# Kernel tuning notes

Hardware: AMD Instinct MI355X
Metric: run time of the kernel (lower is better)

The kernel has to match this reference:

```python
import jax, jax.numpy as jnp
import numpy as np

B, N, HID, NH, NREL, E = 4, 1024, 768, 12, 64, 65536
DH = HID // NH  # 64
TOKEN_TYPE = 0  # NodeType.TOKEN.value


def setup_inputs() -> dict:
    key = jax.random.key(0)
    ks = jax.random.split(key, 24)
    s = 0.02
    inp = {}
    inp["node_states"] = jax.random.normal(ks[0], (B, N, HID), jnp.float32)
    eb = jax.random.randint(ks[1], (E,), 0, B)
    eh = jax.random.randint(ks[2], (E,), 0, N)
    et = jax.random.randint(ks[3], (E,), 0, N)
    er = jax.random.randint(ks[4], (E,), 0, NREL)
    inp["edge_indices"] = jnp.stack([eb, eh, et, er]).astype(jnp.int32)
    inp["node_type_ids"] = jax.random.randint(ks[5], (B, N), 0, 3).astype(jnp.int32)
    names = ["Wq", "Wk", "Wv", "Wq_kb", "Wk_kb", "Wv_kb"]
    for i, nm in enumerate(names):
        inp[nm] = jax.random.normal(ks[6 + i], (HID, HID), jnp.float32) * s
        inp["b" + nm[1:]] = jax.random.normal(ks[12 + i], (HID,), jnp.float32) * s
    inp["rel_mats"] = jax.random.normal(ks[18], (NREL, DH, DH), jnp.float32) * s
    edge_emb = jax.random.normal(ks[19], (NREL, HID), jnp.float32) * s
    inp["edge_emb"] = edge_emb.at[0].set(0.0)  # TOKEN_TO_TOKEN_RELATION_ID row zeroed
    return inp


def reference(node_states, edge_indices, node_type_ids,
              Wq, bq, Wk, bk, Wv, bv,
              Wq_kb, bq_kb, Wk_kb, bk_kb, Wv_kb, bv_kb,
              rel_mats, edge_emb):
    eb, eh, et, er = edge_indices  # (E,) each
    tok = (node_type_ids == TOKEN_TYPE)[..., None]  # (B, N, 1)

    def dual(W_tok, b_tok, W_kb, b_kb):
        # mask_a * tok_proj(x) + mask_b * kb_proj(x)
        return jnp.where(tok, node_states @ W_tok.T + b_tok,
                         node_states @ W_kb.T + b_kb)

    Q = dual(Wq, bq, Wq_kb, bq_kb)  # (B, N, HID)
    K = dual(Wk, bk, Wk_kb, bk_kb)
    V = dual(Wv, bv, Wv_kb, bv_kb)

    # --- attention logits on edges ---
    Qe = Q[eb, eh].reshape(E, NH, DH)  # query at head node
    Ke = K[eb, et].reshape(E, NH, DH)  # key at tail node
    Me = rel_mats[er]                  # (E, DH, DH) per-edge relation matrix
    # (Q @ M) . K per head, scaled
    logits = jnp.einsum('ehd,edf,ehf->eh', Qe, Me, Ke) / jnp.sqrt(
        jnp.asarray(DH, node_states.dtype))  # (E, NH)

    # --- sparse softmax over tail nodes, per (batch, head_node, att_head) ---
    seg = eb * N + eh  # (E,)
    mx = jax.ops.segment_max(logits, seg, num_segments=B * N)  # (B*N, NH)
    ex = jnp.exp(logits - mx[seg])
    denom = jax.ops.segment_sum(ex, seg, num_segments=B * N)
    probs = ex / denom[seg]  # (E, NH); dropout p=0.0 (eval)

    # --- values: V at tail node + edge value embedding ---
    Ve = (V[eb, et] + edge_emb[er]).reshape(E, NH, DH)

    # --- weighted scatter-sum over tail dim ---
    msg = probs[..., None] * Ve  # (E, NH, DH)
    out = jax.ops.segment_sum(msg, seg, num_segments=B * N)  # (B*N, NH, DH)
    return out.reshape(B, N, HID)
```

## Files before the change

kernel.cpp:

```cpp
#include <hip/hip_runtime.h>
#include <math.h>
#include <stdint.h>

#define BB   4
#define NN   1024
#define HID  768
#define NH   12
#define DH   64
#define NREL 64
#define EE   65536
#define NSEG (BB*NN)
#define NOUT 4608
#define UNIT_E 64
#define MAXU (EE/UNIT_E + NREL)
#define NBLK 256
#define MAXMT 34

typedef __bf16 bf16;
typedef __bf16 bf16x8 __attribute__((ext_vector_type(8)));
typedef float  f32x4  __attribute__((ext_vector_type(4)));

__device__ __forceinline__ void load_lds16(const void* g, void* l) {
  __builtin_amdgcn_global_load_lds(
      (__attribute__((address_space(1))) void*)(uintptr_t)g,
      (__attribute__((address_space(3))) void*)(uintptr_t)l, 16, 0, 0);
}

__device__ __forceinline__ int swz(int byte_off) {
  return byte_off ^ (((byte_off >> 7) & 7) << 4);
}

__device__ __forceinline__ float b2f(unsigned short u) {
  return __uint_as_float(((unsigned)u) << 16);
}

__global__ __launch_bounds__(1024)
void partition_kernel(const int* __restrict__ nt, int* __restrict__ origrow,
                      int* __restrict__ meta){
  __shared__ int sums[1024];
  __shared__ int ntot;
  const int t = threadIdx.x;
  int tk[4]; int c = 0;
  #pragma unroll
  for (int i=0;i<4;i++){ tk[i] = (nt[t*4+i]==0); c += tk[i]; }
  sums[t]=c; __syncthreads();
  for (int off=1; off<1024; off<<=1){
    const int v = (t>=off) ? sums[t-off] : 0;
    __syncthreads();
    sums[t]+=v;
    __syncthreads();
  }
  if (t==1023) ntot = sums[1023];
  __syncthreads();
  const int excl = sums[t]-c;
  int tokpos = excl, kbpos = ntot + (4*t - excl);
  #pragma unroll
  for (int i=0;i<4;i++){
    if (tk[i]) origrow[tokpos++] = t*4+i;
    else       origrow[kbpos++]  = t*4+i;
  }
  if (t==0){
    const int ntok = ntot, nkb = NSEG - ntok;
    const int tt = (ntok+127)>>7, ktt = (nkb+127)>>7;
    meta[0]=ntok; meta[1]=tt+ktt;
    for (int m=0;m<tt+ktt;m++){
      meta[2+m]  = (m<tt) ? m*128 : ntok + (m-tt)*128;
      meta[40+m] = (m<tt) ? 1 : 0;
    }
  }
}

__global__ __launch_bounds__(256)
void prep_kernel(const float* __restrict__ X, const int* __restrict__ origrow,
                 const float* __restrict__ W0, const float* __restrict__ W1,
                 const float* __restrict__ W2, const float* __restrict__ W3,
                 const float* __restrict__ W4, const float* __restrict__ W5,
                 const float* __restrict__ b0, const float* __restrict__ b1,
                 const float* __restrict__ b2, const float* __restrict__ b3,
                 const float* __restrict__ b4, const float* __restrict__ b5,
                 const float* __restrict__ relm,
                 bf16* __restrict__ Xp, bf16* __restrict__ Wb,
                 float* __restrict__ biasAll, bf16* __restrict__ Mt){
  const int blk = blockIdx.x, tid = threadIdx.x;
  if (blk < NSEG) {
    if (tid < 192) {
      const int orig = origrow[blk];
      float4 v = *reinterpret_cast<const float4*>(X + (size_t)orig*HID + tid*4);
      bf16 o[4] = {(bf16)v.x,(bf16)v.y,(bf16)v.z,(bf16)v.w};
      *reinterpret_cast<uint64_t*>(Xp + (size_t)blk*HID + tid*4) = *reinterpret_cast<uint64_t*>(o);
    }
  } else if (blk < NSEG + NOUT) {
    const int r = blk - NSEG;
    const int j = r / HID;
    const int o = r - j * HID;
    const float* Wj; const float* bj;
    if      (j==0){Wj=W0;bj=b0;} else if(j==1){Wj=W1;bj=b1;}
    else if (j==2){Wj=W2;bj=b2;} else if(j==3){Wj=W3;bj=b3;}
    else if (j==4){Wj=W4;bj=b4;} else            {Wj=W5;bj=b5;}
    const float* src = Wj + (size_t)o * HID;
    bf16* dst = Wb + (size_t)r * HID;
    for (int c = tid; c < HID; c += 256) dst[c] = (bf16)src[c];
    if (tid == 0) biasAll[r] = bj[o];
  } else {
    const int r = blk - NSEG - NOUT;
    const float* M = relm + (size_t)r * DH * DH;
    bf16* o = Mt + (size_t)r * DH * DH;
    for (int i = tid; i < DH * DH; i += 256) {
      const int d = i >> 6, f = i & 63;
      o[f * DH + d] = (bf16)M[i];
    }
  }
}

#define BM 128
#define BN 128
#define BK 32
#define NT (HID/BK)

__global__ __launch_bounds__(256)
void gemm_kernel(const bf16* __restrict__ A, const bf16* __restrict__ Bw,
                 const float* __restrict__ biasAll, const int* __restrict__ origrow,
                 const int* __restrict__ meta,
                 bf16* __restrict__ Qb, bf16* __restrict__ Kb, bf16* __restrict__ Vb)
{
  __shared__ bf16 As[2][BM * BK];
  __shared__ bf16 Bs[2][BN * BK];
  const int mt = blockIdx.x;
  const int ntok = meta[0], nmt = meta[1];
  if (mt >= nmt) return;
  const int base  = meta[2+mt];
  const int istok = meta[40+mt];

  const int tid  = threadIdx.x;
  const int lane = tid & 63;
  const int w    = tid >> 6;
  const int wrow = w >> 1, wcol = w & 1;
  const int ct_local = blockIdx.y * BN;
  const int brow0 = (istok ? 0 : 2304) + ct_local;

  f32x4 acc[4][4];
  #pragma unroll
  for (int mi=0;mi<4;mi++)
    #pragma unroll
    for (int ni=0;ni<4;ni++) acc[mi][ni] = (f32x4){0.f,0.f,0.f,0.f};

  const char* Ab = (const char*)A;
  const char* Bb = (const char*)Bw;

  int rowg[2], inrowg[2], Pg[2];
  #pragma unroll
  for (int i = 0; i < 2; ++i) {
    const int e = i * 256 + tid;
    const int P = e * 16;
    const int L = swz(P);
    Pg[i] = P; rowg[i] = L >> 6; inrowg[i] = L & 63;
  }

  #define STAGE(kt, b)                                                              \
    { _Pragma("unroll")                                                             \
      for (int i = 0; i < 2; ++i) {                                                 \
        load_lds16(Ab + ((size_t)(base  + rowg[i]) * HID + (kt) * BK) * 2 + inrowg[i], \
                   (char*)As[b] + Pg[i]);                                           \
        load_lds16(Bb + ((size_t)(brow0 + rowg[i]) * HID + (kt) * BK) * 2 + inrowg[i], \
                   (char*)Bs[b] + Pg[i]);                                           \
      } }

  STAGE(0, 0);

  for (int kt = 0; kt < NT; ++kt) {
    __syncthreads();
    if (kt + 1 < NT) STAGE(kt + 1, (kt + 1) & 1);

    const char* Asb = (const char*)As[kt & 1];
    const char* Bsb = (const char*)Bs[kt & 1];
    bf16x8 af[4], bfr[4];
    #pragma unroll
    for (int mi = 0; mi < 4; ++mi) {
      const int r = wrow * 64 + mi * 16 + (lane & 15);
      const int L = r * 64 + (lane >> 4) * 16;
      af[mi] = *reinterpret_cast<const bf16x8*>(Asb + swz(L));
    }
    #pragma unroll
    for (int ni = 0; ni < 4; ++ni) {
      const int r = wcol * 64 + ni * 16 + (lane & 15);
      const int L = r * 64 + (lane >> 4) * 16;
      bfr[ni] = *reinterpret_cast<const bf16x8*>(Bsb + swz(L));
    }
    #pragma unroll
    for (int mi = 0; mi < 4; ++mi)
      #pragma unroll
      for (int ni = 0; ni < 4; ++ni)
        acc[mi][ni] = __builtin_amdgcn_mfma_f32_16x16x32_bf16(af[mi], bfr[ni], acc[mi][ni], 0, 0, 0);
  }

  const int j3 = ct_local / HID;
  const int o0 = ct_local - j3 * HID;
  const int rowLim = istok ? ntok : NSEG;
  const int bidx0 = (istok ? j3 : j3 + 3) * HID + o0;
  #pragma unroll
  for (int mi = 0; mi < 4; ++mi) {
    #pragma unroll
    for (int i = 0; i < 4; ++i) {
      const int rr = base + wrow * 64 + mi * 16 + (lane >> 4) * 4 + i;
      if (rr < rowLim) {
        const int orig = origrow[rr];
        #pragma unroll
        for (int ni = 0; ni < 4; ++ni) {
          const int cg = wcol * 64 + ni * 16 + (lane & 15);
          const float val = acc[mi][ni][i] + biasAll[bidx0 + cg];
          if (j3 == 2)      Vb[(size_t)orig * HID + o0 + cg] = (bf16)val;
          else if (j3 == 0) Qb[(size_t)orig * HID + o0 + cg] = (bf16)val;
          else              Kb[(size_t)orig * HID + o0 + cg] = (bf16)val;
        }
      }
    }
  }
}

__global__ __launch_bounds__(256)
void hist_both_kernel(const int* __restrict__ ei, int* __restrict__ cnt,
                      int* __restrict__ cnt_blk){
  __shared__ int lc[NREL];
  const int tid = threadIdx.x, blk = blockIdx.x;
  if (tid < NREL) lc[tid] = 0;
  __syncthreads();
  const int e = blk*256 + tid;
  atomicAdd(&cnt[ei[e]*NN + ei[EE+e]], 1);
  atomicAdd(&lc[ei[3*EE+e]], 1);
  __syncthreads();
  if (tid < NREL) cnt_blk[tid*NBLK + blk] = lc[tid];
}

__global__ __launch_bounds__(1024)
void scan_both_kernel(const int* __restrict__ cnt, int* __restrict__ start,
                      int* __restrict__ cursor, int* __restrict__ cnt_blk,
                      int* __restrict__ start_rel, int* __restrict__ cnt_rel,
                      int* __restrict__ ustart){
  __shared__ int sums[1024];
  const int t = threadIdx.x;
  if (blockIdx.x == 0) {
    const int c0=cnt[t*4], c1=cnt[t*4+1], c2=cnt[t*4+2], c3=cnt[t*4+3];
    const int s = c0+c1+c2+c3;
    sums[t]=s; __syncthreads();
    for (int off=1; off<1024; off<<=1){
      const int v = (t>=off) ? sums[t-off] : 0;
      __syncthreads();
      sums[t]+=v;
      __syncthreads();
    }
    const int excl = sums[t]-s;
    const int o0=excl, o1=o0+c0, o2=o1+c1, o3=o2+c2;
    start[t*4]=o0;  start[t*4+1]=o1;  start[t*4+2]=o2;  start[t*4+3]=o3;
    cursor[t*4]=o0; cursor[t*4+1]=o1; cursor[t*4+2]=o2; cursor[t*4+3]=o3;
  } else {
    int v[16]; int s = 0;
    #pragma unroll
    for (int i=0;i<16;i++){ v[i] = cnt_blk[t*16+i]; s += v[i]; }
    sums[t] = s; __syncthreads();
    for (int off=1; off<1024; off<<=1){
      const int x = (t>=off) ? sums[t-off] : 0;
      __syncthreads();
      sums[t] += x;
      __syncthreads();
    }
    int run = sums[t] - s;
    #pragma unroll
    for (int i=0;i<16;i++){ const int c = v[i]; cnt_blk[t*16+i] = run; run += c; }
    __syncthreads();
    if (t < NREL) {
      const int st  = cnt_blk[t*NBLK];
      const int nxt = (t == NREL-1) ? EE : cnt_blk[(t+1)*NBLK];
      const int c   = nxt - st;
      start_rel[t] = st;
      cnt_rel[t]   = c;
      const int units = (c + UNIT_E - 1) / UNIT_E;
      int su = units;
      #pragma unroll
      for (int off=1; off<64; off<<=1) {
        const int vu = __shfl_up(su, off);
        if (t >= off) su += vu;
      }
      ustart[t] = su - units;
      if (t == NREL-1) ustart[NREL] = su;
    }
  }
}

__global__ __launch_bounds__(256)
void scatter_both_kernel(const int* __restrict__ ei, int* __restrict__ cursor,
                         int* __restrict__ order, const int* __restrict__ base_blk,
                         int* __restrict__ order_rel){
  __shared__ int lc[NREL];
  const int tid = threadIdx.x, blk = blockIdx.x;
  if (tid < NREL) lc[tid] = 0;
  __syncthreads();
  const int e = blk*256 + tid;
  const int seg = ei[e]*NN + ei[EE+e];
  order[atomicAdd(&cursor[seg], 1)] = e;
  const int r = ei[3*EE + e];
  const int rank = atomicAdd(&lc[r], 1);
  order_rel[base_blk[r*NBLK + blk] + rank] = e;
}

__global__ __launch_bounds__(256)
void logits_mfma_kernel(const bf16* __restrict__ Qb, const bf16* __restrict__ Kb,
                        const int* __restrict__ ei, const bf16* __restrict__ Mt,
                        const int* __restrict__ order_rel, const int* __restrict__ start_rel,
                        const int* __restrict__ cnt_rel, const int* __restrict__ ustart,
                        float* __restrict__ L)
{
  __shared__ int qoff[UNIT_E], koff[UNIT_E], eidx[UNIT_E];
  __shared__ int us[NREL+1];
  __shared__ int relsh;
  const int tid = threadIdx.x;
  const int u = blockIdx.x;
  if (tid < NREL+1) us[tid] = ustart[tid];
  __syncthreads();
  if (u >= us[NREL]) return;
  if (tid < NREL && us[tid] <= u && u < us[tid+1]) relsh = tid;
  __syncthreads();
  const int r = relsh;
  const int lu = u - us[r];
  const int ebase = start_rel[r] + lu * UNIT_E;
  const int nvalid = min(UNIT_E, cnt_rel[r] - lu * UNIT_E);
  if (tid < UNIT_E) {
    const int epos = ebase + (tid < nvalid ? tid : 0);
    const int e = order_rel[epos];
    eidx[tid] = (tid < nvalid) ? e : -1;
    const int eb = ei[e], eh = ei[EE+e], et = ei[2*EE+e];
    qoff[tid] = (eb*NN + eh) * HID;
    koff[tid] = (eb*NN + et) * HID;
  }
  __syncthreads();

  const int w = tid >> 6, lane = tid & 63;
  const int l15 = lane & 15, lg = lane >> 4;
  const bf16* Mr = Mt + (size_t)r * DH * DH;
  bf16x8 bfr[4][2];
  #pragma unroll
  for (int ni = 0; ni < 4; ++ni)
    #pragma unroll
    for (int kk = 0; kk < 2; ++kk)
      bfr[ni][kk] = *reinterpret_cast<const bf16x8*>(
          Mr + (ni*16 + l15) * DH + kk*32 + lg*8);

  #define LOADQ(mt, a0, a1)                                              \
    { const int lr = (mt)*16 + l15;                                      \
      const int el = lr / 12, hh = lr - el*12;                           \
      const int qo = qoff[w*16 + el] + hh*64 + lg*8;                     \
      a0 = *reinterpret_cast<const bf16x8*>(Qb + qo);                    \
      a1 = *reinterpret_cast<const bf16x8*>(Qb + qo + 32); }

  #define LOADK(mt, kr)                                                  \
    { _Pragma("unroll")                                                  \
      for (int i = 0; i < 4; ++i) {                                      \
        const int lr2 = (mt)*16 + lg*4 + i;                              \
        const int el2 = lr2 / 12, h2 = lr2 - el2*12;                     \
        const int ko = koff[w*16 + el2] + h2*64 + l15;                   \
        _Pragma("unroll")                                                \
        for (int ni = 0; ni < 4; ++ni)                                   \
          kr[i*4+ni] = *reinterpret_cast<const unsigned short*>(Kb + ko + ni*16); } }

  #define COMPUTE(mt, a0, a1, kr)                                        \
    { f32x4 acc_[4];                                                     \
      _Pragma("unroll")                                                  \
      for (int ni = 0; ni < 4; ++ni) {                                   \
        acc_[ni] = (f32x4){0.f,0.f,0.f,0.f};                             \
        acc_[ni] = __builtin_amdgcn_mfma_f32_16x16x32_bf16(a0, bfr[ni][0], acc_[ni], 0, 0, 0); \
        acc_[ni] = __builtin_amdgcn_mfma_f32_16x16x32_bf16(a1, bfr[ni][1], acc_[ni], 0, 0, 0); \
      }                                                                  \
      _Pragma("unroll")                                                  \
      for (int i = 0; i < 4; ++i) {                                      \
        const int lr2 = (mt)*16 + lg*4 + i;                              \
        const int el2 = lr2 / 12, h2 = lr2 - el2*12;                     \
        float p = acc_[0][i]*b2f(kr[i*4+0]) + acc_[1][i]*b2f(kr[i*4+1])  \
                + acc_[2][i]*b2f(kr[i*4+2]) + acc_[3][i]*b2f(kr[i*4+3]); \
        p += __shfl_xor(p, 1); p += __shfl_xor(p, 2);                    \
        p += __shfl_xor(p, 4); p += __shfl_xor(p, 8);                    \
        if (l15 == 0) {                                                  \
          const int e = eidx[w*16 + el2];                                \
          if (e >= 0) L[(size_t)e*NH + h2] = p * 0.125f;                 \
        } } }

  bf16x8 a0A, a1A, a0B, a1B;
  unsigned short krA[16], krB[16];
  LOADQ(0, a0A, a1A); LOADK(0, krA);
  #pragma unroll
  for (int mt = 0; mt < 12; mt += 2) {
    LOADQ(mt+1, a0B, a1B); LOADK(mt+1, krB);
    COMPUTE(mt, a0A, a1A, krA);
    if (mt + 2 < 12) { LOADQ(mt+2, a0A, a1A); LOADK(mt+2, krA); }
    COMPUTE(mt+1, a0B, a1B, krB);
  }
  #undef LOADQ
  #undef LOADK
  #undef COMPUTE
}

#define SEGCAP 128
__global__ __launch_bounds__(256)
void segout_kernel(const int* __restrict__ ei, const bf16* __restrict__ Vb,
                   const float* __restrict__ emb, const float* __restrict__ L,
                   const int* __restrict__ start, const int* __restrict__ cnt,
                   const int* __restrict__ order, float* __restrict__ out)
{
  const int s = blockIdx.x, tid = threadIdx.x;
  float* o = out + (size_t)s*HID;
  const int n = cnt[s];
  if (n==0){ o[tid]=0.f; o[tid+256]=0.f; o[tid+512]=0.f; return; }

  __shared__ float denom[NH];
  __shared__ float inv[NH];
  const int st = start[s];
  const int eb = s >> 10;
  const int h0 = tid >> 6;

  if (tid<NH) denom[tid]=0.f;

  if (n <= SEGCAP) {
    __shared__ float pr[SEGCAP*NH];
    __shared__ int voffs[SEGCAP];
    __shared__ int eoffs[SEGCAP];
    if (tid < n) {
      const int e = order[st + tid];
      voffs[tid] = (eb*NN + ei[2*EE+e]) * HID;
      eoffs[tid] = ei[3*EE+e] * HID;
    }
    __syncthreads();
    for (int idx=tid; idx<n*NH; idx+=256){
      const int e = order[st + idx/NH];
      const float v = expf(L[(size_t)e*NH + idx - (idx/NH)*NH]);
      pr[idx] = v;
      atomicAdd(&denom[idx - (idx/NH)*NH], v);
    }
    __syncthreads();
    if (tid<NH) inv[tid] = 1.f/denom[tid];
    __syncthreads();
    const float i0=inv[h0], i1=inv[h0+4], i2=inv[h0+8];
    float a0=0.f, a1=0.f, a2=0.f;
    for (int i=0;i<n;i++){
      const bf16* vr = Vb + voffs[i];
      const float* erow = emb + eoffs[i];
      const float p0 = pr[i*NH+h0  ]*i0;
      const float p1 = pr[i*NH+h0+4]*i1;
      const float p2 = pr[i*NH+h0+8]*i2;
      a0 += p0*(b2f(*(const unsigned short*)(vr+tid    ))+erow[tid    ]);
      a1 += p1*(b2f(*(const unsigned short*)(vr+tid+256))+erow[tid+256]);
      a2 += p2*(b2f(*(const unsigned short*)(vr+tid+512))+erow[tid+512]);
    }
    o[tid]=a0; o[tid+256]=a1; o[tid+512]=a2;
  } else {
    __syncthreads();
    for (int i=tid; i<n*NH; i+=256){
      const int e = order[st + i/NH];
      atomicAdd(&denom[i - (i/NH)*NH], expf(L[(size_t)e*NH + i - (i/NH)*NH]));
    }
    __syncthreads();
    if (tid<NH) inv[tid] = 1.f/denom[tid];
    __syncthreads();
    const float i0=inv[h0], i1=inv[h0+4], i2=inv[h0+8];
    float a0=0.f, a1=0.f, a2=0.f;
    for (int i=0;i<n;i++){
      const int e  = order[st+i];
      const int et = ei[2*EE+e], er = ei[3*EE+e];
      const bf16* vr = Vb + (size_t)(eb*NN+et)*HID;
      const float* erow = emb + (size_t)er*HID;
      const float p0 = expf(L[(size_t)e*NH+h0  ])*i0;
      const float p1 = expf(L[(size_t)e*NH+h0+4])*i1;
      const float p2 = expf(L[(size_t)e*NH+h0+8])*i2;
      a0 += p0*(b2f(*(const unsigned short*)(vr+tid    ))+erow[tid    ]);
      a1 += p1*(b2f(*(const unsigned short*)(vr+tid+256))+erow[tid+256]);
      a2 += p2*(b2f(*(const unsigned short*)(vr+tid+512))+erow[tid+512]);
    }
    o[tid]=a0; o[tid+256]=a1; o[tid+512]=a2;
  }
}

extern "C" void kernel_launch(void* const* d_in, const int* in_sizes, int n_in,
                              void* d_out, int out_size, void* d_ws, size_t ws_size,
                              hipStream_t stream)
{
  const float* X  = (const float*)d_in[0];
  const int*   ei = (const int*)d_in[1];
  const int*   nt = (const int*)d_in[2];
  const float* W[6]; const float* bia[6];
  for (int j=0;j<6;j++){ W[j]=(const float*)d_in[3+2*j]; bia[j]=(const float*)d_in[4+2*j]; }
  const float* relm = (const float*)d_in[15];
  const float* emb  = (const float*)d_in[16];
  float* out = (float*)d_out;

  char* p = (char*)d_ws;
  bf16*  Qb = (bf16*)p;  p += (size_t)NSEG*HID*2;
  bf16*  Kb = (bf16*)p;  p += (size_t)NSEG*HID*2;
  bf16*  Vb = (bf16*)p;  p += (size_t)NSEG*HID*2;
  float* L  = (float*)p; p += (size_t)EE*NH*4;
  int* cnt      = (int*)p; p += NSEG*4;
  int* start    = (int*)p; p += NSEG*4;
  int* cursor   = (int*)p; p += NSEG*4;
  int* order    = (int*)p; p += (size_t)EE*4;
  int* cnt_blk    = (int*)p; p += NREL*NBLK*4;
  int* start_rel  = (int*)p; p += NREL*4;
  int* cnt_rel    = (int*)p; p += NREL*4;
  int* ustart     = (int*)p; p += (NREL+4)*4;
  int* order_rel  = (int*)p; p += (size_t)EE*4;
  int* origrow    = (int*)p; p += (NSEG+128)*4;
  int* meta       = (int*)p; p += 80*4;
  bf16* Xp = (bf16*)p;  p += (size_t)(NSEG+128)*HID*2;
  bf16* Wb = (bf16*)p;  p += (size_t)NOUT*HID*2;
  bf16* Mt = (bf16*)p;  p += (size_t)NREL*DH*DH*2;
  float* biasAll = (float*)p; p += NOUT*4;

  hipMemsetAsync(cnt, 0, NSEG*sizeof(int), stream);

  partition_kernel<<<1, 1024, 0, stream>>>(nt, origrow, meta);
  prep_kernel<<<NSEG + NOUT + NREL, 256, 0, stream>>>(X, origrow,
      W[0],W[1],W[2],W[3],W[4],W[5],
      bia[0],bia[1],bia[2],bia[3],bia[4],bia[5], relm, Xp, Wb, biasAll, Mt);
  gemm_kernel<<<dim3(MAXMT, 2304/BN), 256, 0, stream>>>(Xp, Wb, biasAll, origrow,
      meta, Qb, Kb, Vb);

  hist_both_kernel<<<NBLK, 256, 0, stream>>>(ei, cnt, cnt_blk);
  scan_both_kernel<<<2, 1024, 0, stream>>>(cnt, start, cursor, cnt_blk,
      start_rel, cnt_rel, ustart);
  scatter_both_kernel<<<NBLK, 256, 0, stream>>>(ei, cursor, order, cnt_blk, order_rel);

  logits_mfma_kernel<<<MAXU, 256, 0, stream>>>(Qb, Kb, ei, Mt, order_rel,
      start_rel, cnt_rel, ustart, L);
  segout_kernel<<<NSEG, 256, 0, stream>>>(ei, Vb, emb, L, start, cnt, order, out);
}
```

Before: 149.4 us.

## Shrink GEMM N-tile, fold cnt memset into partition, store edge embeddings as bf16

```diff
diff --git a/kernel.cpp b/kernel.cpp
--- a/kernel.cpp
+++ b/kernel.cpp
@@ -36,13 +36,13 @@
 
 __global__ __launch_bounds__(1024)
 void partition_kernel(const int* __restrict__ nt, int* __restrict__ origrow,
-                      int* __restrict__ meta){
+                      int* __restrict__ meta, int* __restrict__ cnt){
   __shared__ int sums[1024];
   __shared__ int ntot;
   const int t = threadIdx.x;
   int tk[4]; int c = 0;
   #pragma unroll
-  for (int i=0;i<4;i++){ tk[i] = (nt[t*4+i]==0); c += tk[i]; }
+  for (int i=0;i<4;i++){ tk[i] = (nt[t*4+i]==0); c += tk[i]; cnt[t*4+i] = 0; }
   sums[t]=c; __syncthreads();
   for (int off=1; off<1024; off<<=1){
     const int v = (t>=off) ? sums[t-off] : 0;
@@ -78,9 +78,10 @@
                  const float* __restrict__ b0, const float* __restrict__ b1,
                  const float* __restrict__ b2, const float* __restrict__ b3,
                  const float* __restrict__ b4, const float* __restrict__ b5,
-                 const float* __restrict__ relm,
+                 const float* __restrict__ relm, const float* __restrict__ emb,
                  bf16* __restrict__ Xp, bf16* __restrict__ Wb,
-                 float* __restrict__ biasAll, bf16* __restrict__ Mt){
+                 float* __restrict__ biasAll, bf16* __restrict__ Mt,
+                 bf16* __restrict__ Eb){
   const int blk = blockIdx.x, tid = threadIdx.x;
   if (blk < NSEG) {
     if (tid < 192) {
@@ -101,7 +102,7 @@
     bf16* dst = Wb + (size_t)r * HID;
     for (int c = tid; c < HID; c += 256) dst[c] = (bf16)src[c];
     if (tid == 0) biasAll[r] = bj[o];
-  } else {
+  } else if (blk < NSEG + NOUT + NREL) {
     const int r = blk - NSEG - NOUT;
     const float* M = relm + (size_t)r * DH * DH;
     bf16* o = Mt + (size_t)r * DH * DH;
@@ -109,11 +110,16 @@
       const int d = i >> 6, f = i & 63;
       o[f * DH + d] = (bf16)M[i];
     }
+  } else {
+    const int r = blk - NSEG - NOUT - NREL;
+    const float* src = emb + (size_t)r * HID;
+    bf16* dst = Eb + (size_t)r * HID;
+    for (int c = tid; c < HID; c += 256) dst[c] = (bf16)src[c];
   }
 }
 
 #define BM 128
-#define BN 128
+#define BN 64
 #define BK 32
 #define NT (HID/BK)
 
@@ -138,32 +144,33 @@
   const int ct_local = blockIdx.y * BN;
   const int brow0 = (istok ? 0 : 2304) + ct_local;
 
-  f32x4 acc[4][4];
+  f32x4 acc[4][2];
   #pragma unroll
   for (int mi=0;mi<4;mi++)
     #pragma unroll
-    for (int ni=0;ni<4;ni++) acc[mi][ni] = (f32x4){0.f,0.f,0.f,0.f};
+    for (int ni=0;ni<2;ni++) acc[mi][ni] = (f32x4){0.f,0.f,0.f,0.f};
 
   const char* Ab = (const char*)A;
   const char* Bb = (const char*)Bw;
 
-  int rowg[2], inrowg[2], Pg[2];
+  int rowgA[2], inrowgA[2], PgA[2];
   #pragma unroll
   for (int i = 0; i < 2; ++i) {
-    const int e = i * 256 + tid;
-    const int P = e * 16;
+    const int P = (i * 256 + tid) * 16;
     const int L = swz(P);
-    Pg[i] = P; rowg[i] = L >> 6; inrowg[i] = L & 63;
-  }
+    PgA[i] = P; rowgA[i] = L >> 6; inrowgA[i] = L & 63;
+  }
+  const int PB = tid * 16;
+  const int LB = swz(PB);
+  const int rowgB = LB >> 6, inrowgB = LB & 63;
 
   #define STAGE(kt, b)                                                              \
     { _Pragma("unroll")                                                             \
-      for (int i = 0; i < 2; ++i) {                                                 \
-        load_lds16(Ab + ((size_t)(base  + rowg[i]) * HID + (kt) * BK) * 2 + inrowg[i], \
-                   (char*)As[b] + Pg[i]);                                           \
-        load_lds16(Bb + ((size_t)(brow0 + rowg[i]) * HID + (kt) * BK) * 2 + inrowg[i], \
-                   (char*)Bs[b] + Pg[i]);                                           \
-      } }
+      for (int i = 0; i < 2; ++i)                                                   \
+        load_lds16(Ab + ((size_t)(base  + rowgA[i]) * HID + (kt) * BK) * 2 + inrowgA[i], \
+                   (char*)As[b] + PgA[i]);                                          \
+      load_lds16(Bb + ((size_t)(brow0 + rowgB) * HID + (kt) * BK) * 2 + inrowgB,    \
+                 (char*)Bs[b] + PB); }
 
   STAGE(0, 0);
 
@@ -173,7 +180,7 @@
 
     const char* Asb = (const char*)As[kt & 1];
     const char* Bsb = (const char*)Bs[kt & 1];
-    bf16x8 af[4], bfr[4];
+    bf16x8 af[4], bfr[2];
     #pragma unroll
     for (int mi = 0; mi < 4; ++mi) {
       const int r = wrow * 64 + mi * 16 + (lane & 15);
@@ -181,15 +188,15 @@
       af[mi] = *reinterpret_cast<const bf16x8*>(Asb + swz(L));
     }
     #pragma unroll
-    for (int ni = 0; ni < 4; ++ni) {
-      const int r = wcol * 64 + ni * 16 + (lane & 15);
+    for (int ni = 0; ni < 2; ++ni) {
+      const int r = wcol * 32 + ni * 16 + (lane & 15);
       const int L = r * 64 + (lane >> 4) * 16;
       bfr[ni] = *reinterpret_cast<const bf16x8*>(Bsb + swz(L));
     }
     #pragma unroll
     for (int mi = 0; mi < 4; ++mi)
       #pragma unroll
-      for (int ni = 0; ni < 4; ++ni)
+      for (int ni = 0; ni < 2; ++ni)
         acc[mi][ni] = __builtin_amdgcn_mfma_f32_16x16x32_bf16(af[mi], bfr[ni], acc[mi][ni], 0, 0, 0);
   }
 
@@ -205,8 +212,8 @@
       if (rr < rowLim) {
         const int orig = origrow[rr];
         #pragma unroll
-        for (int ni = 0; ni < 4; ++ni) {
-          const int cg = wcol * 64 + ni * 16 + (lane & 15);
+        for (int ni = 0; ni < 2; ++ni) {
+          const int cg = wcol * 32 + ni * 16 + (lane & 15);
           const float val = acc[mi][ni][i] + biasAll[bidx0 + cg];
           if (j3 == 2)      Vb[(size_t)orig * HID + o0 + cg] = (bf16)val;
           else if (j3 == 0) Qb[(size_t)orig * HID + o0 + cg] = (bf16)val;
@@ -400,7 +407,7 @@
 #define SEGCAP 128
 __global__ __launch_bounds__(256)
 void segout_kernel(const int* __restrict__ ei, const bf16* __restrict__ Vb,
-                   const float* __restrict__ emb, const float* __restrict__ L,
+                   const bf16* __restrict__ Eb, const float* __restrict__ L,
                    const int* __restrict__ start, const int* __restrict__ cnt,
                    const int* __restrict__ order, float* __restrict__ out)
 {
@@ -440,13 +447,13 @@
     float a0=0.f, a1=0.f, a2=0.f;
     for (int i=0;i<n;i++){
       const bf16* vr = Vb + voffs[i];
-      const float* erow = emb + eoffs[i];
+      const bf16* erow = Eb + eoffs[i];
       const float p0 = pr[i*NH+h0  ]*i0;
       const float p1 = pr[i*NH+h0+4]*i1;
       const float p2 = pr[i*NH+h0+8]*i2;
-      a0 += p0*(b2f(*(const unsigned short*)(vr+tid    ))+erow[tid    ]);
-      a1 += p1*(b2f(*(const unsigned short*)(vr+tid+256))+erow[tid+256]);
-      a2 += p2*(b2f(*(const unsigned short*)(vr+tid+512))+erow[tid+512]);
+      a0 += p0*(b2f(*(const unsigned short*)(vr+tid    ))+b2f(*(const unsigned short*)(erow+tid    )));
+      a1 += p1*(b2f(*(const unsigned short*)(vr+tid+256))+b2f(*(const unsigned short*)(erow+tid+256)));
+      a2 += p2*(b2f(*(const unsigned short*)(vr+tid+512))+b2f(*(const unsigned short*)(erow+tid+512)));
     }
     o[tid]=a0; o[tid+256]=a1; o[tid+512]=a2;
   } else {
@@ -464,13 +471,13 @@
       const int e  = order[st+i];
       const int et = ei[2*EE+e], er = ei[3*EE+e];
       const bf16* vr = Vb + (size_t)(eb*NN+et)*HID;
-      const float* erow = emb + (size_t)er*HID;
+      const bf16* erow = Eb + (size_t)er*HID;
       const float p0 = expf(L[(size_t)e*NH+h0  ])*i0;
       const float p1 = expf(L[(size_t)e*NH+h0+4])*i1;
       const float p2 = expf(L[(size_t)e*NH+h0+8])*i2;
-      a0 += p0*(b2f(*(const unsigned short*)(vr+tid    ))+erow[tid    ]);
-      a1 += p1*(b2f(*(const unsigned short*)(vr+tid+256))+erow[tid+256]);
-      a2 += p2*(b2f(*(const unsigned short*)(vr+tid+512))+erow[tid+512]);
+      a0 += p0*(b2f(*(const unsigned short*)(vr+tid    ))+b2f(*(const unsigned short*)(erow+tid    )));
+      a1 += p1*(b2f(*(const unsigned short*)(vr+tid+256))+b2f(*(const unsigned short*)(erow+tid+256)));
+      a2 += p2*(b2f(*(const unsigned short*)(vr+tid+512))+b2f(*(const unsigned short*)(erow+tid+512)));
     }
     o[tid]=a0; o[tid+256]=a1; o[tid+512]=a2;
   }
@@ -508,14 +515,13 @@
   bf16* Xp = (bf16*)p;  p += (size_t)(NSEG+128)*HID*2;
   bf16* Wb = (bf16*)p;  p += (size_t)NOUT*HID*2;
   bf16* Mt = (bf16*)p;  p += (size_t)NREL*DH*DH*2;
+  bf16* Eb = (bf16*)p;  p += (size_t)NREL*HID*2;
   float* biasAll = (float*)p; p += NOUT*4;
 
-  hipMemsetAsync(cnt, 0, NSEG*sizeof(int), stream);
-
-  partition_kernel<<<1, 1024, 0, stream>>>(nt, origrow, meta);
-  prep_kernel<<<NSEG + NOUT + NREL, 256, 0, stream>>>(X, origrow,
+  partition_kernel<<<1, 1024, 0, stream>>>(nt, origrow, meta, cnt);
+  prep_kernel<<<NSEG + NOUT + NREL + NREL, 256, 0, stream>>>(X, origrow,
       W[0],W[1],W[2],W[3],W[4],W[5],
-      bia[0],bia[1],bia[2],bia[3],bia[4],bia[5], relm, Xp, Wb, biasAll, Mt);
+      bia[0],bia[1],bia[2],bia[3],bia[4],bia[5], relm, emb, Xp, Wb, biasAll, Mt, Eb);
   gemm_kernel<<<dim3(MAXMT, 2304/BN), 256, 0, stream>>>(Xp, Wb, biasAll, origrow,
       meta, Qb, Kb, Vb);
 
@@ -526,5 +532,5 @@
 
   logits_mfma_kernel<<<MAXU, 256, 0, stream>>>(Qb, Kb, ei, Mt, order_rel,
       start_rel, cnt_rel, ustart, L);
-  segout_kernel<<<NSEG, 256, 0, stream>>>(ei, Vb, emb, L, start, cnt, order, out);
-}
+  segout_kernel<<<NSEG, 256, 0, stream>>>(ei, Vb, Eb, L, start, cnt, order, out);
+}
```

Result: no change. 151.2 us (+1.2%).
